# Performance work log

Hardware: AMD Instinct MI355X
Metric: run time of the kernel (lower is better)

The kernel has to match this reference:

```python
import jax, jax.numpy as jnp
import numpy as np

B, C, H, W = 16, 256, 64, 64
P, HEADS, D = 8, 8, 32  # window size, heads, channels per head


def setup_inputs() -> dict:
    key = jax.random.key(0)
    k1, k2, k3, k4 = jax.random.split(key, 4)
    x = jax.random.normal(k1, (B, C, H, W), jnp.float32)
    # kaiming-ish init for the 1x1 convs (stored as [out, in] matrices)
    w_proj = jax.random.normal(k2, (3 * HEADS * D, C), jnp.float32) * (2.0 / C) ** 0.5
    # original inits position to zeros; use small noise so the bias path is exercised
    position = jax.random.normal(k3, (HEADS, 2 * P, 2 * P), jnp.float32) * 0.02
    w_out = jax.random.normal(k4, (C, HEADS * D), jnp.float32) * (2.0 / (HEADS * D)) ** 0.5
    b_out = jnp.zeros((C,), jnp.float32)
    return {"x": x, "w_proj": w_proj, "position": position, "w_out": w_out, "b_out": b_out}


def _rel_bias(position):
    # unfolded_posenc: relative offsets between all pairs of positions in a PxP window
    coords = jnp.stack(jnp.meshgrid(jnp.arange(P), jnp.arange(P), indexing="ij"), -1).reshape(P * P, 2)
    rel = coords[None, :, :] - coords[:, None, :] + P  # [P^2, P^2, 2], values in [1, 2P-1]
    return position[:, rel[..., 0], rel[..., 1]]  # [heads, P^2, P^2]


def reference(x, w_proj, position, w_out, b_out):
    b, c, h, w = x.shape
    nh, nw = h // P, w // P
    # 1x1 conv projection to qkv: [B, 3*heads*D, H, W]
    qkv = jnp.einsum("bchw,oc->bohw", x, w_proj)
    # window partition -> [3, B, heads, nh, nw, P*P, D]
    qkv = qkv.reshape(b, 3, HEADS, D, nh, P, nw, P)
    qkv = qkv.transpose(1, 0, 2, 4, 6, 5, 7, 3).reshape(3, b, HEADS, nh, nw, P * P, D)
    q, k, v = qkv[0], qkv[1], qkv[2]
    bias = _rel_bias(position)  # [heads, P^2, P^2]
    scale = 1.0 / jnp.sqrt(jnp.asarray(D, x.dtype))
    scores = jnp.einsum("bhnmqd,bhnmkd->bhnmqk", q, k) * scale + bias[None, :, None, None]
    attn = jax.nn.softmax(scores, axis=-1)
    o = jnp.einsum("bhnmqk,bhnmkd->bhnmqd", attn, v)  # [B, heads, nh, nw, P^2, D]
    # fold windows back to [B, heads*D, H, W]
    o = o.reshape(b, HEADS, nh, nw, P, P, D)
    o = o.transpose(0, 1, 6, 2, 4, 3, 5).reshape(b, HEADS * D, h, w)
    # output 1x1 conv with bias
    return jnp.einsum("bchw,oc->bohw", o, w_out) + b_out[None, :, None, None]
```

## Files before the change

kernel.cpp:

```cpp
#include <hip/hip_runtime.h>


typedef _Float16 f16x8 __attribute__((ext_vector_type(8)));
typedef float    f32x4 __attribute__((ext_vector_type(4)));
typedef unsigned short u16;
typedef unsigned long long u64;

#define SCALE 0.17677669529663687f
#define QK_S  40
#define VT_S  72
#define PB_S  40
#define LT_S  264
#define XW_S  264

__device__ __forceinline__ u16 f2hu(float f) {
    _Float16 h = (_Float16)f; return __builtin_bit_cast(u16, h);
}
__device__ __forceinline__ u64 pack4h(f32x4 v) {
    return (u64)f2hu(v[0]) | ((u64)f2hu(v[1]) << 16)
         | ((u64)f2hu(v[2]) << 32) | ((u64)f2hu(v[3]) << 48);
}

__global__ __launch_bounds__(512)
void prep(const float* __restrict__ x, const float* __restrict__ wp,
          const float* __restrict__ wo, u16* __restrict__ xtw,
          u16* __restrict__ w16k, u16* __restrict__ wo16k)
{
    __shared__ u16 Lt[64 * LT_S];
    const int bid = blockIdx.x;
    const int tid = threadIdx.x;
    if (bid < 1024) {
        const int y = bid & 63, b = bid >> 6;
        const int yq = y >> 3, py = y & 7;
        const float* xb = x + ((size_t)b * 256) * 4096 + y * 64;
        #pragma unroll
        for (int i = 0; i < 8; ++i) {
            int idx = tid + i * 512;
            int c = idx >> 4, w4 = (idx & 15) << 2;
            float4 v = *(const float4*)(xb + (size_t)c * 4096 + w4);
            float vv[4] = {v.x, v.y, v.z, v.w};
            #pragma unroll
            for (int j = 0; j < 4; ++j) {
                int w = w4 + j;
                Lt[w * LT_S + (c ^ (((w >> 2) & 7) << 3))] = f2hu(vv[j]);
            }
        }
        __syncthreads();
        u16* dst = xtw + (size_t)(b * 64 + yq * 8) * 16384;
        #pragma unroll
        for (int i = 0; i < 4; ++i) {
            int idx = tid + i * 512;
            int w = idx >> 5, c8 = (idx & 31) << 3;
            f16x8 v = *(const f16x8*)(&Lt[w * LT_S + (c8 ^ (((w >> 2) & 7) << 3))]);
            *(f16x8*)(dst + (w >> 3) * 16384 + (py * 8 + (w & 7)) * 256 + c8) = v;
        }
    } else {
        int idx = (bid - 1024) * 512 + tid;
        if (idx < 196608) {
            int hq = idx / 98304, o = idx - hq * 98304;
            int kt = o / 12288, o2 = o - kt * 12288;
            int lr = o2 >> 5, cc = o2 & 31;
            int s = lr >> 7, hh = (lr >> 5) & 3, d = lr & 31;
            w16k[idx] = f2hu(wp[(size_t)(s * 256 + (hq * 4 + hh) * 32 + d) * 256 + kt * 32 + cc]);
        } else {
            int j = idx - 196608;
            int kt = j >> 13, o2 = j & 8191;
            int row = o2 >> 5, cc = o2 & 31;
            wo16k[j] = f2hu(wo[(size_t)row * 256 + kt * 32 + cc]);
        }
    }
}

__global__ __launch_bounds__(512, 4)
void lsa_qkv_attn_xt(const u16* __restrict__ xtw, const u16* __restrict__ w16k,
                     const float* __restrict__ position, u16* __restrict__ Ows)
{
    __shared__ u16 U[29696];
    __shared__ float POSL[2048];
    u16* XwL = U;
    u16* Qb  = U;
    u16* Kb  = U + 10240;
    u16* Vt  = U + 20480;

    const int tid = threadIdx.x;
    const int hq = blockIdx.x & 1, win = blockIdx.x >> 1, b = blockIdx.y;
    const int w = tid >> 6, m = tid & 15, lg = (tid >> 4) & 3;

    *(float4*)(&POSL[tid * 4]) = *(const float4*)(position + tid * 4);
    {
        const u16* xwin = xtw + (size_t)(b * 64 + win) * 16384;
        #pragma unroll
        for (int i = 0; i < 4; ++i) {
            int g = tid + i * 512;
            *(f16x8*)(XwL + (g >> 5) * XW_S + (g & 31) * 8) = *(const f16x8*)(xwin + g * 8);
        }
    }
    __syncthreads();

    f32x4 acc[3][4];
    int isv[3], hhv[3], d0v[3], lr0v[3];
    {
        const f32x4 z = {0.f, 0.f, 0.f, 0.f};
        #pragma unroll
        for (int i = 0; i < 3; ++i) {
            #pragma unroll
            for (int nt = 0; nt < 4; ++nt) acc[i][nt] = z;
            int lr0 = (3 * w + i) * 16;
            lr0v[i] = lr0;
            isv[i] = lr0 >> 7; hhv[i] = (lr0 >> 5) & 3; d0v[i] = lr0 & 31;
        }
        const u16* wbase = w16k + (size_t)hq * 98304;
        #pragma unroll
        for (int kt = 0; kt < 8; ++kt) {
            f16x8 af[3], bf[4];
            #pragma unroll
            for (int i = 0; i < 3; ++i)
                af[i] = *(const f16x8*)(wbase + kt * 12288 + (lr0v[i] + m) * 32 + lg * 8);
            #pragma unroll
            for (int nt = 0; nt < 4; ++nt)
                bf[nt] = *(const f16x8*)(XwL + (nt * 16 + m) * XW_S + kt * 32 + lg * 8);
            #pragma unroll
            for (int i = 0; i < 3; ++i)
                #pragma unroll
                for (int nt = 0; nt < 4; ++nt)
                    acc[i][nt] = __builtin_amdgcn_mfma_f32_16x16x32_f16(af[i], bf[nt], acc[i][nt], 0, 0, 0);
        }
    }
    __syncthreads();

    {
        #pragma unroll
        for (int i = 0; i < 3; ++i) {
            int i_s = isv[i], hh = hhv[i], d0 = d0v[i];
            #pragma unroll
            for (int nt = 0; nt < 4; ++nt) {
                int pix = nt * 16 + m;
                if (i_s < 2) {
                    u16* base = (i_s == 0) ? Qb : Kb;
                    *(u64*)(base + hh * 64 * QK_S + pix * QK_S + d0 + lg * 4) = pack4h(acc[i][nt]);
                } else {
                    #pragma unroll
                    for (int r = 0; r < 4; ++r)
                        Vt[hh * 32 * VT_S + (d0 + lg * 4 + r) * VT_S + pix] = f2hu(acc[i][nt][r]);
                }
            }
        }
    }
    __syncthreads();

    {
        const int hh = w >> 1, qh = w & 1;
        const u16* Qh = Qb + hh * 64 * QK_S;
        const u16* Kh = Kb + hh * 64 * QK_S;
        const u16* Vh = Vt + hh * 32 * VT_S;
        u16* Ph = Qb + hh * 64 * PB_S;
        const float* posh = &POSL[(hq * 4 + hh) * 256];

        f16x8 kf[4], qf[2];
        #pragma unroll
        for (int kt = 0; kt < 4; ++kt)
            kf[kt] = *(const f16x8*)(Kh + (kt * 16 + m) * QK_S + lg * 8);
        #pragma unroll
        for (int qi = 0; qi < 2; ++qi)
            qf[qi] = *(const f16x8*)(Qh + ((2 * qh + qi) * 16 + m) * QK_S + lg * 8);
        __syncthreads();

        const f32x4 z = {0.f, 0.f, 0.f, 0.f};
        f32x4 st[4][2];
        #pragma unroll
        for (int kt = 0; kt < 4; ++kt)
            #pragma unroll
            for (int qi = 0; qi < 2; ++qi)
                st[kt][qi] = __builtin_amdgcn_mfma_f32_16x16x32_f16(kf[kt], qf[qi], z, 0, 0, 0);

        float inv[2];
        #pragma unroll
        for (int qi = 0; qi < 2; ++qi) {
            int q = (2 * qh + qi) * 16 + m, qy = q >> 3, qx = q & 7;
            float mx = -1e30f;
            #pragma unroll
            for (int kt = 0; kt < 4; ++kt)
                #pragma unroll
                for (int r = 0; r < 4; ++r) {
                    int k = kt * 16 + lg * 4 + r, ky = k >> 3, kx = k & 7;
                    float t = st[kt][qi][r] * SCALE + posh[(ky - qy + 8) * 16 + (kx - qx + 8)];
                    st[kt][qi][r] = t;
                    mx = fmaxf(mx, t);
                }
            mx = fmaxf(mx, __shfl_xor(mx, 16));
            mx = fmaxf(mx, __shfl_xor(mx, 32));
            float sum = 0.f;
            #pragma unroll
            for (int kt = 0; kt < 4; ++kt)
                #pragma unroll
                for (int r = 0; r < 4; ++r) {
                    float e = __expf(st[kt][qi][r] - mx);
                    st[kt][qi][r] = e; sum += e;
                }
            sum += __shfl_xor(sum, 16);
            sum += __shfl_xor(sum, 32);
            inv[qi] = 1.f / sum;
        }

        f32x4 ot[2][2];
        ot[0][0] = z; ot[0][1] = z; ot[1][0] = z; ot[1][1] = z;
        #pragma unroll
        for (int ks = 0; ks < 2; ++ks) {
            #pragma unroll
            for (int kh = 0; kh < 2; ++kh) {
                int kt = 2 * ks + kh;
                #pragma unroll
                for (int qi = 0; qi < 2; ++qi) {
                    f32x4 pv = st[kt][qi] * inv[qi];
                    *(u64*)(Ph + ((2 * qh + qi) * 16 + m) * PB_S + kh * 16 + lg * 4) = pack4h(pv);
                }
            }
            f16x8 pf[2], vf[2];
            #pragma unroll
            for (int qi = 0; qi < 2; ++qi)
                pf[qi] = *(const f16x8*)(Ph + ((2 * qh + qi) * 16 + m) * PB_S + lg * 8);
            #pragma unroll
            for (int dt = 0; dt < 2; ++dt)
                vf[dt] = *(const f16x8*)(Vh + (dt * 16 + m) * VT_S + ks * 32 + lg * 8);
            #pragma unroll
            for (int qi = 0; qi < 2; ++qi)
                #pragma unroll
                for (int dt = 0; dt < 2; ++dt)
                    ot[qi][dt] = __builtin_amdgcn_mfma_f32_16x16x32_f16(pf[qi], vf[dt], ot[qi][dt], 0, 0, 0);
        }

        const size_t obase = (size_t)(b * 64 + win) * 16384;
        const int head = hq * 4 + hh;
        #pragma unroll
        for (int qi = 0; qi < 2; ++qi)
            #pragma unroll
            for (int dt = 0; dt < 2; ++dt) {
                int c = head * 32 + dt * 16 + m;
                #pragma unroll
                for (int r = 0; r < 4; ++r) {
                    int q = (2 * qh + qi) * 16 + lg * 4 + r;
                    Ows[obase + q * 256 + c] = f2hu(ot[qi][dt][r]);
                }
            }
    }
}

__global__ __launch_bounds__(512, 4)
void lsa_outproj(const u16* __restrict__ Ows, const u16* __restrict__ wo16k,
                 const float* __restrict__ b_out, float* __restrict__ out)
{
    __shared__ u16 Owt[64 * XW_S];

    const int tid = threadIdx.x;
    const int win = blockIdx.x, b = blockIdx.y;
    const int wy = win >> 3, wx = win & 7;
    const int w = tid >> 6, m = tid & 15, lg = (tid >> 4) & 3;

    {
        const u16* Ow = Ows + (size_t)(b * 64 + win) * 16384;
        #pragma unroll
        for (int i = 0; i < 4; ++i) {
            int g = tid + i * 512;
            *(f16x8*)(Owt + (g >> 5) * XW_S + (g & 31) * 8) = *(const f16x8*)(Ow + g * 8);
        }
    }
    __syncthreads();

    f32x4 oa[2][4];
    {
        const f32x4 z = {0.f, 0.f, 0.f, 0.f};
        #pragma unroll
        for (int mt = 0; mt < 2; ++mt)
            #pragma unroll
            for (int nt = 0; nt < 4; ++nt) oa[mt][nt] = z;
    }
    #pragma unroll
    for (int kt = 0; kt < 8; ++kt) {
        f16x8 wf[2], of[4];
        #pragma unroll
        for (int mt = 0; mt < 2; ++mt)
            wf[mt] = *(const f16x8*)(wo16k + kt * 8192 + (w * 32 + mt * 16 + m) * 32 + lg * 8);
        #pragma unroll
        for (int nt = 0; nt < 4; ++nt)
            of[nt] = *(const f16x8*)(Owt + (nt * 16 + m) * XW_S + kt * 32 + lg * 8);
        #pragma unroll
        for (int mt = 0; mt < 2; ++mt)
            #pragma unroll
            for (int nt = 0; nt < 4; ++nt)
                oa[mt][nt] = __builtin_amdgcn_mfma_f32_16x16x32_f16(wf[mt], of[nt], oa[mt][nt], 0, 0, 0);
    }
    float* ob = out + ((size_t)b * 256) * 4096 + (wy * 8) * 64 + wx * 8;
    #pragma unroll
    for (int mt = 0; mt < 2; ++mt)
        #pragma unroll
        for (int nt = 0; nt < 4; ++nt) {
            int p = nt * 16 + m, py = p >> 3, px = p & 7;
            #pragma unroll
            for (int r = 0; r < 4; ++r) {
                int oc = w * 32 + mt * 16 + lg * 4 + r;
                ob[(size_t)oc * 4096 + py * 64 + px] = oa[mt][nt][r] + b_out[oc];
            }
        }
}

extern "C" void kernel_launch(void* const* d_in, const int* in_sizes, int n_in,
                              void* d_out, int out_size, void* d_ws, size_t ws_size,
                              hipStream_t stream) {
    const float* x      = (const float*)d_in[0];
    const float* w_proj = (const float*)d_in[1];
    const float* pos    = (const float*)d_in[2];
    const float* w_out  = (const float*)d_in[3];
    const float* b_out  = (const float*)d_in[4];
    float* out = (float*)d_out;

    u16* xtw   = (u16*)d_ws;
    u16* w16k  = (u16*)((char*)d_ws + 33554432);
    u16* wo16k = (u16*)((char*)d_ws + 33554432 + 393216);
    u16* Ows   = (u16*)((char*)d_ws + 33554432 + 393216 + 131072);

    prep<<<1536, 512, 0, stream>>>(x, w_proj, w_out, xtw, w16k, wo16k);
    lsa_qkv_attn_xt<<<dim3(128, 16), 512, 0, stream>>>(xtw, w16k, pos, Ows);
    lsa_outproj<<<dim3(64, 16), 512, 0, stream>>>(Ows, wo16k, b_out, out);
}
```

Baseline: 102.4 us.

## Tile output projection by image rows for coalesced stores; trim position staging

The output projection now gives each block one image row (64 pixels across 8 windows) instead of one 8x8 window. Each warp's fp32 stores then cover 16 contiguous pixels rather than 8-pixel fragments, while reads from the window-ordered intermediate are gathered from 8 windows. The attention kernel also loads only the half of the position table its head group uses, which halves that shared array. Packing to fp16 now uses the round-toward-zero pack instruction instead of four scalar converts, which slightly changes rounding.

```diff
diff --git a/kernel.cpp b/kernel.cpp
--- a/kernel.cpp
+++ b/kernel.cpp
@@ -2,8 +2,10 @@
 
 
 typedef _Float16 f16x8 __attribute__((ext_vector_type(8)));
+typedef __fp16   fp16x2 __attribute__((ext_vector_type(2)));
 typedef float    f32x4 __attribute__((ext_vector_type(4)));
 typedef unsigned short u16;
+typedef unsigned int   u32;
 typedef unsigned long long u64;
 
 #define SCALE 0.17677669529663687f
@@ -12,13 +14,15 @@
 #define PB_S  40
 #define LT_S  264
 #define XW_S  264
+#define OT_S  264
 
 __device__ __forceinline__ u16 f2hu(float f) {
     _Float16 h = (_Float16)f; return __builtin_bit_cast(u16, h);
 }
 __device__ __forceinline__ u64 pack4h(f32x4 v) {
-    return (u64)f2hu(v[0]) | ((u64)f2hu(v[1]) << 16)
-         | ((u64)f2hu(v[2]) << 32) | ((u64)f2hu(v[3]) << 48);
+    u32 lo = __builtin_bit_cast(u32, __builtin_amdgcn_cvt_pkrtz(v[0], v[1]));
+    u32 hi = __builtin_bit_cast(u32, __builtin_amdgcn_cvt_pkrtz(v[2], v[3]));
+    return ((u64)hi << 32) | (u64)lo;
 }
 
 __global__ __launch_bounds__(512)
@@ -76,7 +80,7 @@
                      const float* __restrict__ position, u16* __restrict__ Ows)
 {
     __shared__ u16 U[29696];
-    __shared__ float POSL[2048];
+    __shared__ float POSL[1024];
     u16* XwL = U;
     u16* Qb  = U;
     u16* Kb  = U + 10240;
@@ -86,7 +90,7 @@
     const int hq = blockIdx.x & 1, win = blockIdx.x >> 1, b = blockIdx.y;
     const int w = tid >> 6, m = tid & 15, lg = (tid >> 4) & 3;
 
-    *(float4*)(&POSL[tid * 4]) = *(const float4*)(position + tid * 4);
+    *(float2*)(&POSL[tid * 2]) = *(const float2*)(position + hq * 1024 + tid * 2);
     {
         const u16* xwin = xtw + (size_t)(b * 64 + win) * 16384;
         #pragma unroll
@@ -154,7 +158,7 @@
         const u16* Kh = Kb + hh * 64 * QK_S;
         const u16* Vh = Vt + hh * 32 * VT_S;
         u16* Ph = Qb + hh * 64 * PB_S;
-        const float* posh = &POSL[(hq * 4 + hh) * 256];
+        const float* posh = &POSL[hh * 256];
 
         f16x8 kf[4], qf[2];
         #pragma unroll
@@ -246,22 +250,25 @@
 }
 
 __global__ __launch_bounds__(512, 4)
-void lsa_outproj(const u16* __restrict__ Ows, const u16* __restrict__ wo16k,
-                 const float* __restrict__ b_out, float* __restrict__ out)
+void lsa_outproj_row(const u16* __restrict__ Ows, const u16* __restrict__ wo16k,
+                     const float* __restrict__ b_out, float* __restrict__ out)
 {
-    __shared__ u16 Owt[64 * XW_S];
+    __shared__ u16 Ot[64 * OT_S];
 
     const int tid = threadIdx.x;
-    const int win = blockIdx.x, b = blockIdx.y;
-    const int wy = win >> 3, wx = win & 7;
+    const int y = blockIdx.x, b = blockIdx.y;
+    const int yq = y >> 3, py = y & 7;
     const int w = tid >> 6, m = tid & 15, lg = (tid >> 4) & 3;
 
     {
-        const u16* Ow = Ows + (size_t)(b * 64 + win) * 16384;
+        const u16* slab = Ows + (size_t)(b * 64 + yq * 8) * 16384 + (py * 8) * 256;
         #pragma unroll
         for (int i = 0; i < 4; ++i) {
             int g = tid + i * 512;
-            *(f16x8*)(Owt + (g >> 5) * XW_S + (g & 31) * 8) = *(const f16x8*)(Ow + g * 8);
+            int wx = g >> 8, gg = g & 255;
+            int lx = gg >> 5, c8 = (gg & 31) << 3;
+            f16x8 v = *(const f16x8*)(slab + (size_t)wx * 16384 + lx * 256 + c8);
+            *(f16x8*)(Ot + (wx * 8 + lx) * OT_S + c8) = v;
         }
     }
     __syncthreads();
@@ -282,23 +289,23 @@
             wf[mt] = *(const f16x8*)(wo16k + kt * 8192 + (w * 32 + mt * 16 + m) * 32 + lg * 8);
         #pragma unroll
         for (int nt = 0; nt < 4; ++nt)
-            of[nt] = *(const f16x8*)(Owt + (nt * 16 + m) * XW_S + kt * 32 + lg * 8);
+            of[nt] = *(const f16x8*)(Ot + (nt * 16 + m) * OT_S + kt * 32 + lg * 8);
         #pragma unroll
         for (int mt = 0; mt < 2; ++mt)
             #pragma unroll
             for (int nt = 0; nt < 4; ++nt)
                 oa[mt][nt] = __builtin_amdgcn_mfma_f32_16x16x32_f16(wf[mt], of[nt], oa[mt][nt], 0, 0, 0);
     }
-    float* ob = out + ((size_t)b * 256) * 4096 + (wy * 8) * 64 + wx * 8;
+    float* ob = out + (size_t)b * 1048576 + y * 64;
     #pragma unroll
     for (int mt = 0; mt < 2; ++mt)
         #pragma unroll
         for (int nt = 0; nt < 4; ++nt) {
-            int p = nt * 16 + m, py = p >> 3, px = p & 7;
+            int px = nt * 16 + m;
             #pragma unroll
             for (int r = 0; r < 4; ++r) {
                 int oc = w * 32 + mt * 16 + lg * 4 + r;
-                ob[(size_t)oc * 4096 + py * 64 + px] = oa[mt][nt][r] + b_out[oc];
+                ob[(size_t)oc * 4096 + px] = oa[mt][nt][r] + b_out[oc];
             }
         }
 }
@@ -320,5 +327,5 @@
 
     prep<<<1536, 512, 0, stream>>>(x, w_proj, w_out, xtw, w16k, wo16k);
     lsa_qkv_attn_xt<<<dim3(128, 16), 512, 0, stream>>>(xtw, w16k, pos, Ows);
-    lsa_outproj<<<dim3(64, 16), 512, 0, stream>>>(Ows, wo16k, b_out, out);
-}
+    lsa_outproj_row<<<dim3(64, 16), 512, 0, stream>>>(Ows, wo16k, b_out, out);
+}
```

Result: faster. 89.55 us (-12.5%).
